# Optimization experiments

Measured on AMD Instinct MI355X. Metric: run time of the kernel, lower is better.

Reference implementation:

```python
import jax, jax.numpy as jnp
import numpy as np

NUM_HEADS = 16
HEAD_SIZE = 64
MAX_POS = 2048  # config.max_position_embeddings


def setup_inputs() -> dict:
    key = jax.random.key(0)
    ks = jax.random.split(key, 8)
    B, Lq, Lk, D = 4, 1024, 2048, 1024
    s = 1.0 / np.sqrt(D)
    return {
        "hidden_states": jax.random.normal(ks[0], (B, Lk, D), jnp.float32),
        "query_hidden_states": jax.random.normal(ks[1], (B, Lq, D), jnp.float32),
        "attention_mask": jnp.zeros((B, 1, 1, Lk), jnp.float32),
        "Wq": jax.random.normal(ks[2], (D, D), jnp.float32) * s,
        "bq": jnp.zeros((D,), jnp.float32),
        "Wk": jax.random.normal(ks[3], (D, D), jnp.float32) * s,
        "bk": jnp.zeros((D,), jnp.float32),
        "Wv": jax.random.normal(ks[4], (D, D), jnp.float32) * s,
        "bv": jnp.zeros((D,), jnp.float32),
        "dist_emb": jax.random.normal(ks[5], (2 * MAX_POS - 1, HEAD_SIZE), jnp.float32) * 0.02,
    }


def _split_heads(x):
    # [B, L, H*Dh] -> [B, H, L, Dh]
    B, L, _ = x.shape
    return x.reshape(B, L, NUM_HEADS, HEAD_SIZE).transpose(0, 2, 1, 3)


def reference(hidden_states, query_hidden_states, attention_mask, Wq, bq, Wk, bk, Wv, bv, dist_emb):
    # Linear projections (torch Linear: x @ W.T + b)
    q = _split_heads(query_hidden_states @ Wq.T + bq)   # [B,H,Lq,Dh]
    k = _split_heads(hidden_states @ Wk.T + bk)          # [B,H,Lk,Dh]
    v = _split_heads(hidden_states @ Wv.T + bv)          # [B,H,Lk,Dh]

    scores = jnp.einsum('bhld,bhrd->bhlr', q, k)         # [B,H,Lq,Lk]

    # relative_key_query positional scores
    Lq, Lk = q.shape[2], k.shape[2]
    distance = jnp.arange(Lq)[:, None] - jnp.arange(Lk)[None, :]
    pe = dist_emb[distance + MAX_POS - 1]                # [Lq,Lk,Dh]
    scores = scores + jnp.einsum('bhld,lrd->bhlr', q, pe) + jnp.einsum('bhrd,lrd->bhlr', k, pe)

    scores = scores / np.sqrt(HEAD_SIZE) + attention_mask
    probs = jax.nn.softmax(scores, axis=-1)              # dropout p=0 (eval)
    ctx = jnp.einsum('bhlr,bhrd->bhld', probs, v)        # [B,H,Lq,Dh]
    B = ctx.shape[0]
    return ctx.transpose(0, 2, 1, 3).reshape(B, Lq, NUM_HEADS * HEAD_SIZE)
```

## Files before the change

### kernel.cpp

```cpp
#include <hip/hip_runtime.h>
#include <hip/hip_bf16.h>

#define B_   4
#define H_   16
#define LQ   1024
#define LK   2048
#define D_   1024
#define DH   64

typedef __attribute__((ext_vector_type(8))) short  short8;
typedef __attribute__((ext_vector_type(4))) float  float4_;
typedef __attribute__((ext_vector_type(4))) unsigned int uint4_;

static __device__ __forceinline__ float bf2f(unsigned short u) {
    unsigned int x = ((unsigned int)u) << 16;
    return __builtin_bit_cast(float, x);
}
static __device__ __forceinline__ unsigned short f2bf(float f) {
    unsigned int x = __builtin_bit_cast(unsigned int, f);
    unsigned int lsb = (x >> 16) & 1u;
    x += 0x7fffu + lsb;
    return (unsigned short)(x >> 16);
}
static __device__ __forceinline__ unsigned int pack2(float a, float b) {
    __hip_bfloat162 h = __float22bfloat162_rn(make_float2(a, b));
    unsigned int r;
    __builtin_memcpy(&r, &h, 4);
    return r;
}

#define MFMA(a, b, c) __builtin_amdgcn_mfma_f32_16x16x32_bf16((a), (b), (c), 0, 0, 0)

#define G2ROW(tl) ((tl) * 144 + ((tl) >> 2) * 8)

#define GLOAD_LDS16(g, l) __builtin_amdgcn_global_load_lds( \
    (const __attribute__((address_space(1))) unsigned int*)(const void*)(g), \
    (__attribute__((address_space(3))) unsigned int*)(void*)(l), 16, 0, 0)

__global__ __launch_bounds__(256) void conv_kernel(
    const float* __restrict__ Wq, const float* __restrict__ Wk,
    const float* __restrict__ Wv, const float* __restrict__ Eg,
    const float* __restrict__ Xq, const float* __restrict__ Xk,
    unsigned short* __restrict__ cWq, unsigned short* __restrict__ cWk,
    unsigned short* __restrict__ cWv, unsigned short* __restrict__ cEb,
    unsigned short* __restrict__ cXq, unsigned short* __restrict__ cXk)
{
    int bid = blockIdx.x;
    const float* src; unsigned short* dst; int nch;
    if (bid < 512)       { src = Wq; dst = cWq;              nch = 131072;  }
    else if (bid < 1024) { src = Wk; dst = cWk; bid -= 512;  nch = 131072;  }
    else if (bid < 1536) { src = Wv; dst = cWv; bid -= 1024; nch = 131072;  }
    else if (bid < 1664) { src = Eg; dst = cEb; bid -= 1536; nch = 32760;   }
    else if (bid < 3712) { src = Xq; dst = cXq; bid -= 1664; nch = 524288;  }
    else                 { src = Xk; dst = cXk; bid -= 3712; nch = 1048576; }
    int ch = bid * 256 + threadIdx.x;
    if (ch >= nch) return;
    const float* s = src + (size_t)ch * 8;
    float4_ v0 = *(const float4_*)s, v1 = *(const float4_*)(s + 4);
    uint4_ o;
    o[0] = pack2(v0[0], v0[1]); o[1] = pack2(v0[2], v0[3]);
    o[2] = pack2(v1[0], v1[1]); o[3] = pack2(v1[2], v1[3]);
    *(uint4_*)(dst + (size_t)ch * 8) = o;
}

__global__ __launch_bounds__(256) void proj_kernel(
    const unsigned short* __restrict__ Xq, const unsigned short* __restrict__ Xk,
    const unsigned short* __restrict__ Wq, const float* __restrict__ bq,
    const unsigned short* __restrict__ Wk, const float* __restrict__ bk,
    const unsigned short* __restrict__ Wv, const float* __restrict__ bv,
    unsigned short* __restrict__ Qh, unsigned short* __restrict__ Kh,
    unsigned short* __restrict__ VT)
{
    __shared__ short smem[17408];
    short* As = smem;
    short* Bs = smem + 8192;
    short* Cs = smem;

    int bid = blockIdx.x;
    int which, tm, tn;
    const unsigned short *X; const float* bias; const unsigned short* W;
    if (bid < 256)      { which = 0; int t = bid;       tm = t >> 3; tn = t & 7; X = Xq; W = Wq; bias = bq; }
    else if (bid < 768) { which = 1; int t = bid - 256; tm = t >> 3; tn = t & 7; X = Xk; W = Wk; bias = bk; }
    else                { which = 2; int t = bid - 768; tm = t >> 3; tn = t & 7; X = Xk; W = Wv; bias = bv; }

    int tid  = threadIdx.x;
    int wave = tid >> 6, lane = tid & 63;
    int wr = (wave >> 1) * 64, wc = (wave & 1) * 64;
    int m0 = tm * 128, n0 = tn * 128;

    float4_ acc[4][4];
    for (int a = 0; a < 4; ++a) for (int c = 0; c < 4; ++c) acc[a][c] = (float4_)0.0f;

    int rl = lane >> 3;
    int chs = (lane & 7) ^ rl;
    const unsigned short* Asrc = X + (size_t)(m0 + wave * 32 + rl) * D_ + (chs << 3);
    const unsigned short* Bsrc = W + (size_t)(n0 + wave * 32 + rl) * D_ + (chs << 3);

    int lrow = lane & 15, lk8 = (lane >> 4) * 8;
    int swz = lane & 7;

    for (int kt = 0; kt < 16; ++kt) {
        int k0 = kt * 64;
        #pragma unroll
        for (int c = 0; c < 4; ++c) {
            GLOAD_LDS16(Asrc + (size_t)(c * 8) * D_ + k0, &As[(wave * 32 + c * 8) * 64]);
            GLOAD_LDS16(Bsrc + (size_t)(c * 8) * D_ + k0, &Bs[(wave * 32 + c * 8) * 64]);
        }
        __syncthreads();
        #pragma unroll
        for (int kk = 0; kk < 64; kk += 32) {
            int cgrp = (kk + lk8) >> 3;
            int coff = ((cgrp ^ swz) << 3);
            short8 af[4], bfr[4];
            #pragma unroll
            for (int rt = 0; rt < 4; ++rt)
                af[rt]  = *(const short8*)(&As[(wr + rt * 16 + lrow) * 64 + coff]);
            #pragma unroll
            for (int ct = 0; ct < 4; ++ct)
                bfr[ct] = *(const short8*)(&Bs[(wc + ct * 16 + lrow) * 64 + coff]);
            #pragma unroll
            for (int rt = 0; rt < 4; ++rt)
                #pragma unroll
                for (int ct = 0; ct < 4; ++ct)
                    acc[rt][ct] = MFMA(af[rt], bfr[ct], acc[rt][ct]);
        }
        __syncthreads();
    }

    int lrow4 = (lane >> 4) * 4, lcol = lane & 15;
    if (which < 2) {
        int lsh = (which == 0) ? 10 : 11;
        int Lm1 = (1 << lsh) - 1;
        unsigned short* dst = (which == 0) ? Qh : Kh;
        for (int rt = 0; rt < 4; ++rt)
            for (int ct = 0; ct < 4; ++ct)
                for (int i = 0; i < 4; ++i) {
                    int m = m0 + wr + rt * 16 + lrow4 + i;
                    int n = n0 + wc + ct * 16 + lcol;
                    float v = acc[rt][ct][i] + bias[n];
                    int b = m >> lsh, s = m & Lm1;
                    int h = n >> 6, d = n & 63;
                    dst[((size_t)((b * H_ + h) << lsh) + (size_t)s) * DH + d] = f2bf(v);
                }
    } else {
        for (int rt = 0; rt < 4; ++rt)
            for (int ct = 0; ct < 4; ++ct)
                for (int i = 0; i < 4; ++i) {
                    int rl2 = wr + rt * 16 + lrow4 + i;
                    int cl  = wc + ct * 16 + lcol;
                    float v = acc[rt][ct][i] + bias[n0 + cl];
                    Cs[cl * 136 + rl2] = (short)f2bf(v);
                }
        __syncthreads();
        int b = m0 >> 11, r0 = m0 & 2047;
        int c = tid >> 1, half = tid & 1;
        int n = n0 + c, h = n >> 6, d = n & 63;
        unsigned short* dstp = VT + ((size_t)(b * H_ + h) * DH + d) * LK + r0 + half * 64;
        for (int j = 0; j < 8; ++j) {
            uint4_ v = *(const uint4_*)(&Cs[c * 136 + half * 64 + j * 8]);
            *(uint4_*)(dstp + j * 8) = v;
        }
    }
}

__global__ __launch_bounds__(256, 2) void attn_kernel(
    const unsigned short* __restrict__ Qh, const unsigned short* __restrict__ Kh,
    const unsigned short* __restrict__ VT, const unsigned short* __restrict__ Eb,
    const float* __restrict__ mask, float* __restrict__ out)
{
    __shared__ short smem[27776];
    short* Qs  = smem;
    short* Ks  = smem;
    short* VTs = smem + 4608;
    short* Es  = smem + 9216;
    short* G2  = smem + 18432;
    short* Ps  = G2;

    int bid = blockIdx.x;
    int l0 = (bid & 15) * 64;
    int bh = bid >> 4;
    int b  = bh >> 4, h = bh & 15;
    int tid = threadIdx.x, wave = tid >> 6, lane = tid & 63;
    int lr = lane & 15, lk8 = (lane >> 4) * 8, lr4 = (lane >> 4) * 4;

    for (int i = 0; i < 2; ++i) {
        int idx = tid + 256 * i, row = idx >> 3, g = (idx & 7) * 8;
        *(uint4_*)(&Qs[row * 72 + g]) =
            *(const uint4_*)(Qh + ((size_t)(bh * LQ + l0 + row)) * DH + g);
    }
    __syncthreads();
    short8 aq0 = *(const short8*)(&Qs[(wave * 16 + lr) * 72 + lk8]);
    short8 aq1 = *(const short8*)(&Qs[(wave * 16 + lr) * 72 + 32 + lk8]);

    float m_i[4], l_i[4];
    float4_ Oacc[4];
    for (int i = 0; i < 4; ++i) { m_i[i] = -1e30f; l_i[i] = 0.f; Oacc[i] = (float4_)0.f; }

    const unsigned short* Kbase = Kh + (size_t)bh * LK * DH;
    const unsigned short* Vbase = VT + (size_t)bh * DH * LK;

    int srow = tid >> 3;
    int sg   = (tid & 7) * 8;

    uint4_ kr0, kr1, vr0, vr1, er0, er1, er2, er3;
    auto load_tiles = [&](int it2) {
        int r0_ = it2 * 64, jb_ = l0 - r0_ + 1984;
        kr0 = *(const uint4_*)(Kbase + (size_t)(r0_ + srow) * DH + sg);
        kr1 = *(const uint4_*)(Kbase + (size_t)(r0_ + srow + 32) * DH + sg);
        vr0 = *(const uint4_*)(Vbase + (size_t)srow * LK + r0_ + sg);
        vr1 = *(const uint4_*)(Vbase + (size_t)(srow + 32) * LK + r0_ + sg);
        er0 = *(const uint4_*)(Eb + (size_t)(jb_ + srow) * DH + sg);
        er1 = *(const uint4_*)(Eb + (size_t)(jb_ + srow + 32) * DH + sg);
        er2 = *(const uint4_*)(Eb + (size_t)(jb_ + srow + 64) * DH + sg);
        er3 = *(const uint4_*)(Eb + (size_t)(jb_ + srow + 96) * DH + sg);
    };
    load_tiles(0);

    for (int it = 0; it < 32; ++it) {
        int r0 = it * 64;

        __syncthreads();
        *(uint4_*)(&Ks[srow * 72 + sg])         = kr0;
        *(uint4_*)(&Ks[(srow + 32) * 72 + sg])  = kr1;
        *(uint4_*)(&VTs[srow * 72 + sg])        = vr0;
        *(uint4_*)(&VTs[(srow + 32) * 72 + sg]) = vr1;
        *(uint4_*)(&Es[srow * 72 + sg])         = er0;
        *(uint4_*)(&Es[(srow + 32) * 72 + sg])  = er1;
        *(uint4_*)(&Es[(srow + 64) * 72 + sg])  = er2;
        *(uint4_*)(&Es[(srow + 96) * 72 + sg])  = er3;
        __syncthreads();
        if (it < 31) load_tiles(it + 1);

        float4_ Sacc[4];
        for (int c = 0; c < 4; ++c) {
            short8 b0 = *(const short8*)(&Ks[(c * 16 + lr) * 72 + lk8]);
            short8 b1 = *(const short8*)(&Ks[(c * 16 + lr) * 72 + 32 + lk8]);
            float4_ s = (float4_)0.f;
            s = MFMA(aq0, b0, s);
            s = MFMA(aq1, b1, s);
            Sacc[c] = s;
        }

        short8 ak0 = *(const short8*)(&Ks[(wave * 16 + lr) * 72 + lk8]);
        short8 ak1 = *(const short8*)(&Ks[(wave * 16 + lr) * 72 + 32 + lk8]);
        unsigned int gqp[5][2], gkp[5][2];
        for (int tt = 0; tt < 5; ++tt) {
            int tqi = wave + tt;
            short8 e0 = *(const short8*)(&Es[(tqi * 16 + lr) * 72 + lk8]);
            short8 e1 = *(const short8*)(&Es[(tqi * 16 + lr) * 72 + 32 + lk8]);
            float4_ g = (float4_)0.f;
            g = MFMA(aq0, e0, g); g = MFMA(aq1, e1, g);
            gqp[tt][0] = pack2(g[0], g[1]); gqp[tt][1] = pack2(g[2], g[3]);
            int tk = (3 - wave) + tt;
            short8 f0 = *(const short8*)(&Es[(tk * 16 + lr) * 72 + lk8]);
            short8 f1 = *(const short8*)(&Es[(tk * 16 + lr) * 72 + 32 + lk8]);
            float4_ gg = (float4_)0.f;
            gg = MFMA(ak0, f0, gg); gg = MFMA(ak1, f1, gg);
            gkp[tt][0] = pack2(gg[0], gg[1]); gkp[tt][1] = pack2(gg[2], gg[3]);
        }

        for (int tt = 0; tt < 5; ++tt) {
            int uq = (wave + tt) * 16 + lr;
            int uk = (3 - wave + tt) * 16 + lr;
            for (int i = 0; i < 4; ++i) {
                int row = wave * 16 + lr4 + i;
                unsigned int wq32 = gqp[tt][i >> 1], wk32 = gkp[tt][i >> 1];
                unsigned short vq = (unsigned short)((i & 1) ? (wq32 >> 16) : (wq32 & 0xffff));
                unsigned short vk = (unsigned short)((i & 1) ? (wk32 >> 16) : (wk32 & 0xffff));
                int tr = row - uq + 63;
                if ((unsigned)tr < 64u)
                    G2[G2ROW(row) + ((tr & 15) << 3) + (((tr >> 4)) << 1)] = (short)vq;
                int tl = uk + row - 63;
                if ((unsigned)tl < 64u)
                    G2[G2ROW(tl) + ((row & 15) << 3) + (((row >> 4)) << 1) + 1] = (short)vk;
            }
        }
        __syncthreads();

        float mk[4];
        for (int c = 0; c < 4; ++c) mk[c] = mask[b * LK + r0 + c * 16 + lr];
        for (int i = 0; i < 4; ++i) {
            int tl = wave * 16 + lr4 + i;
            short8 gv = *(const short8*)(&G2[G2ROW(tl) + (lr << 3)]);
            float scv[4], mx = -1e30f;
            for (int c = 0; c < 4; ++c) {
                float sq = bf2f((unsigned short)gv[2 * c]);
                float sk = bf2f((unsigned short)gv[2 * c + 1]);
                float sc = (Sacc[c][i] + sq + sk) * 0.125f + mk[c];
                scv[c] = sc;
                mx = fmaxf(mx, sc);
            }
            for (int off = 1; off < 16; off <<= 1) mx = fmaxf(mx, __shfl_xor(mx, off, 64));
            float mnew = fmaxf(m_i[i], mx);
            float alpha = __expf(m_i[i] - mnew);
            m_i[i] = mnew;
            float e0 = __expf(scv[0] - mnew), e1 = __expf(scv[1] - mnew);
            float e2 = __expf(scv[2] - mnew), e3 = __expf(scv[3] - mnew);
            unsigned int p01 = pack2(e0, e1), p23 = pack2(e2, e3);
            float rs = bf2f((unsigned short)(p01 & 0xffff)) + bf2f((unsigned short)(p01 >> 16))
                     + bf2f((unsigned short)(p23 & 0xffff)) + bf2f((unsigned short)(p23 >> 16));
            for (int off = 1; off < 16; off <<= 1) rs += __shfl_xor(rs, off, 64);
            l_i[i] = l_i[i] * alpha + rs;
            for (int nt = 0; nt < 4; ++nt) Oacc[nt][i] *= alpha;
            Ps[G2ROW(tl) +  0 + lr] = (short)(unsigned short)(p01 & 0xffff);
            Ps[G2ROW(tl) + 16 + lr] = (short)(unsigned short)(p01 >> 16);
            Ps[G2ROW(tl) + 32 + lr] = (short)(unsigned short)(p23 & 0xffff);
            Ps[G2ROW(tl) + 48 + lr] = (short)(unsigned short)(p23 >> 16);
        }
        short8 ap0 = *(const short8*)(&Ps[G2ROW(wave * 16 + lr) + lk8]);
        short8 ap1 = *(const short8*)(&Ps[G2ROW(wave * 16 + lr) + 32 + lk8]);
        for (int nt = 0; nt < 4; ++nt) {
            short8 v0 = *(const short8*)(&VTs[(nt * 16 + lr) * 72 + lk8]);
            short8 v1 = *(const short8*)(&VTs[(nt * 16 + lr) * 72 + 32 + lk8]);
            Oacc[nt] = MFMA(ap0, v0, Oacc[nt]);
            Oacc[nt] = MFMA(ap1, v1, Oacc[nt]);
        }
    }

    for (int nt = 0; nt < 4; ++nt)
        for (int i = 0; i < 4; ++i) {
            int row = l0 + wave * 16 + lr4 + i;
            int col = h * 64 + nt * 16 + lr;
            out[(size_t)(b * LQ + row) * D_ + col] = Oacc[nt][i] / l_i[i];
        }
}

extern "C" void kernel_launch(void* const* d_in, const int* in_sizes, int n_in,
                              void* d_out, int out_size, void* d_ws, size_t ws_size,
                              hipStream_t stream) {
    (void)in_sizes; (void)n_in; (void)out_size; (void)ws_size;
    const float* Xk   = (const float*)d_in[0];
    const float* Xq   = (const float*)d_in[1];
    const float* mask = (const float*)d_in[2];
    const float* Wq   = (const float*)d_in[3];
    const float* bq   = (const float*)d_in[4];
    const float* Wk   = (const float*)d_in[5];
    const float* bk   = (const float*)d_in[6];
    const float* Wv   = (const float*)d_in[7];
    const float* bv   = (const float*)d_in[8];
    const float* Eg   = (const float*)d_in[9];

    unsigned short* Qh  = (unsigned short*)d_ws;
    unsigned short* Kh  = Qh  + (size_t)4194304;
    unsigned short* VT  = Kh  + (size_t)8388608;
    unsigned short* cWq = VT  + (size_t)8388608;
    unsigned short* cWk = cWq + (size_t)1048576;
    unsigned short* cWv = cWk + (size_t)1048576;
    unsigned short* cEb = cWv + (size_t)1048576;
    unsigned short* cXq = cEb + (size_t)262144;
    unsigned short* cXk = (unsigned short*)d_out;
    float* o = (float*)d_out;

    conv_kernel<<<7808, 256, 0, stream>>>(Wq, Wk, Wv, Eg, Xq, Xk,
                                          cWq, cWk, cWv, cEb, cXq, cXk);
    proj_kernel<<<1280, 256, 0, stream>>>(cXq, cXk, cWq, bq, cWk, bk, cWv, bv, Qh, Kh, VT);
    attn_kernel<<<1024, 256, 0, stream>>>(Qh, Kh, VT, cEb, mask, o);
}
```

Before: 446.1 us.

## Double-buffer projection GEMM LDS tiles and repad attention G2 scratch layout

The projection GEMM now double-buffers its A/B LDS tiles, issuing global-to-LDS loads for the next k-tile while MFMAs run on the current one, so load latency is hidden behind compute. In the attention kernel, the shared relative-position scratch is changed from a swizzled G2ROW layout to a padded 65-word row of packed q/k pairs, and P gets its own padded buffer. The aim is fewer LDS bank conflicts. The cost is that projection LDS use rises to 64KB and attention LDS use grows, which may reduce occupancy.

```diff
diff --git a/kernel.cpp b/kernel.cpp
--- a/kernel.cpp
+++ b/kernel.cpp
@@ -30,8 +30,6 @@
 }
 
 #define MFMA(a, b, c) __builtin_amdgcn_mfma_f32_16x16x32_bf16((a), (b), (c), 0, 0, 0)
-
-#define G2ROW(tl) ((tl) * 144 + ((tl) >> 2) * 8)
 
 #define GLOAD_LDS16(g, l) __builtin_amdgcn_global_load_lds( \
     (const __attribute__((address_space(1))) unsigned int*)(const void*)(g), \
@@ -71,9 +69,11 @@
     unsigned short* __restrict__ Qh, unsigned short* __restrict__ Kh,
     unsigned short* __restrict__ VT)
 {
-    __shared__ short smem[17408];
-    short* As = smem;
-    short* Bs = smem + 8192;
+    __shared__ short smem[32768];
+    short* A0 = smem;
+    short* B0 = smem + 8192;
+    short* A1 = smem + 16384;
+    short* B1 = smem + 24576;
     short* Cs = smem;
 
     int bid = blockIdx.x;
@@ -99,14 +99,15 @@
     int lrow = lane & 15, lk8 = (lane >> 4) * 8;
     int swz = lane & 7;
 
-    for (int kt = 0; kt < 16; ++kt) {
+    auto stage = [&](short* Ad, short* Bd, int kt) {
         int k0 = kt * 64;
         #pragma unroll
         for (int c = 0; c < 4; ++c) {
-            GLOAD_LDS16(Asrc + (size_t)(c * 8) * D_ + k0, &As[(wave * 32 + c * 8) * 64]);
-            GLOAD_LDS16(Bsrc + (size_t)(c * 8) * D_ + k0, &Bs[(wave * 32 + c * 8) * 64]);
-        }
-        __syncthreads();
+            GLOAD_LDS16(Asrc + (size_t)(c * 8) * D_ + k0, &Ad[(wave * 32 + c * 8) * 64]);
+            GLOAD_LDS16(Bsrc + (size_t)(c * 8) * D_ + k0, &Bd[(wave * 32 + c * 8) * 64]);
+        }
+    };
+    auto compute = [&](const short* Aa, const short* Bb) {
         #pragma unroll
         for (int kk = 0; kk < 64; kk += 32) {
             int cgrp = (kk + lk8) >> 3;
@@ -114,16 +115,26 @@
             short8 af[4], bfr[4];
             #pragma unroll
             for (int rt = 0; rt < 4; ++rt)
-                af[rt]  = *(const short8*)(&As[(wr + rt * 16 + lrow) * 64 + coff]);
+                af[rt]  = *(const short8*)(&Aa[(wr + rt * 16 + lrow) * 64 + coff]);
             #pragma unroll
             for (int ct = 0; ct < 4; ++ct)
-                bfr[ct] = *(const short8*)(&Bs[(wc + ct * 16 + lrow) * 64 + coff]);
+                bfr[ct] = *(const short8*)(&Bb[(wc + ct * 16 + lrow) * 64 + coff]);
             #pragma unroll
             for (int rt = 0; rt < 4; ++rt)
                 #pragma unroll
                 for (int ct = 0; ct < 4; ++ct)
                     acc[rt][ct] = MFMA(af[rt], bfr[ct], acc[rt][ct]);
         }
+    };
+
+    stage(A0, B0, 0);
+    __syncthreads();
+    for (int kt = 0; kt < 16; kt += 2) {
+        if (kt + 1 < 16) stage(A1, B1, kt + 1);
+        compute(A0, B0);
+        __syncthreads();
+        if (kt + 2 < 16) stage(A0, B0, kt + 2);
+        compute(A1, B1);
         __syncthreads();
     }
 
@@ -168,13 +179,14 @@
     const unsigned short* __restrict__ VT, const unsigned short* __restrict__ Eb,
     const float* __restrict__ mask, float* __restrict__ out)
 {
-    __shared__ short smem[27776];
+    __shared__ short smem[31360];
     short* Qs  = smem;
     short* Ks  = smem;
     short* VTs = smem + 4608;
     short* Es  = smem + 9216;
-    short* G2  = smem + 18432;
-    short* Ps  = G2;
+    short* Ps  = smem + 18432;
+    unsigned int* Gqk = (unsigned int*)(smem + 23040);
+    short* Gs  = smem + 23040;
 
     int bid = blockIdx.x;
     int l0 = (bid & 15) * 64;
@@ -269,10 +281,10 @@
                 unsigned short vk = (unsigned short)((i & 1) ? (wk32 >> 16) : (wk32 & 0xffff));
                 int tr = row - uq + 63;
                 if ((unsigned)tr < 64u)
-                    G2[G2ROW(row) + ((tr & 15) << 3) + (((tr >> 4)) << 1)] = (short)vq;
+                    Gs[(row * 65 + tr) * 2] = (short)vq;
                 int tl = uk + row - 63;
                 if ((unsigned)tl < 64u)
-                    G2[G2ROW(tl) + ((row & 15) << 3) + (((row >> 4)) << 1) + 1] = (short)vk;
+                    Gs[(tl * 65 + row) * 2 + 1] = (short)vk;
             }
         }
         __syncthreads();
@@ -281,11 +293,14 @@
         for (int c = 0; c < 4; ++c) mk[c] = mask[b * LK + r0 + c * 16 + lr];
         for (int i = 0; i < 4; ++i) {
             int tl = wave * 16 + lr4 + i;
-            short8 gv = *(const short8*)(&G2[G2ROW(tl) + (lr << 3)]);
+            const unsigned int* gr = Gqk + tl * 65 + lr;
+            unsigned int gva[4];
+            gva[0] = gr[0]; gva[1] = gr[16]; gva[2] = gr[32]; gva[3] = gr[48];
             float scv[4], mx = -1e30f;
+            #pragma unroll
             for (int c = 0; c < 4; ++c) {
-                float sq = bf2f((unsigned short)gv[2 * c]);
-                float sk = bf2f((unsigned short)gv[2 * c + 1]);
+                float sq = bf2f((unsigned short)(gva[c] & 0xffff));
+                float sk = bf2f((unsigned short)(gva[c] >> 16));
                 float sc = (Sacc[c][i] + sq + sk) * 0.125f + mk[c];
                 scv[c] = sc;
                 mx = fmaxf(mx, sc);
@@ -302,13 +317,15 @@
             for (int off = 1; off < 16; off <<= 1) rs += __shfl_xor(rs, off, 64);
             l_i[i] = l_i[i] * alpha + rs;
             for (int nt = 0; nt < 4; ++nt) Oacc[nt][i] *= alpha;
-            Ps[G2ROW(tl) +  0 + lr] = (short)(unsigned short)(p01 & 0xffff);
-            Ps[G2ROW(tl) + 16 + lr] = (short)(unsigned short)(p01 >> 16);
-            Ps[G2ROW(tl) + 32 + lr] = (short)(unsigned short)(p23 & 0xffff);
-            Ps[G2ROW(tl) + 48 + lr] = (short)(unsigned short)(p23 >> 16);
-        }
-        short8 ap0 = *(const short8*)(&Ps[G2ROW(wave * 16 + lr) + lk8]);
-        short8 ap1 = *(const short8*)(&Ps[G2ROW(wave * 16 + lr) + 32 + lk8]);
+            short* Pr = Ps + tl * 72;
+            Pr[ 0 + lr] = (short)(unsigned short)(p01 & 0xffff);
+            Pr[16 + lr] = (short)(unsigned short)(p01 >> 16);
+            Pr[32 + lr] = (short)(unsigned short)(p23 & 0xffff);
+            Pr[48 + lr] = (short)(unsigned short)(p23 >> 16);
+        }
+        const short* Pa = Ps + (wave * 16 + lr) * 72;
+        short8 ap0 = *(const short8*)(Pa + lk8);
+        short8 ap1 = *(const short8*)(Pa + 32 + lk8);
         for (int nt = 0; nt < 4; ++nt) {
             short8 v0 = *(const short8*)(&VTs[(nt * 16 + lr) * 72 + lk8]);
             short8 v1 = *(const short8*)(&VTs[(nt * 16 + lr) * 72 + 32 + lk8]);
```

Measured after the change: 425.3 us, median of 3. 4.7% less time.
